# Optimization experiments

Hardware: AMD Instinct MI355X
Metric: run time of the kernel (lower is better)

Reference implementation:

```python
import jax, jax.numpy as jnp
import numpy as np

NUM_EMBEDDINGS = 1024
EMBEDDING_DIM = 256
COMMITMENT_COST = 0.25


def setup_inputs() -> dict:
    key = jax.random.key(0)
    k_z, k_e = jax.random.split(key)
    z = jax.random.normal(k_z, (16, EMBEDDING_DIM, 4096), dtype=jnp.float32)
    # nn.Embedding init: uniform(-1/K, 1/K)
    emb = jax.random.uniform(
        k_e, (NUM_EMBEDDINGS, EMBEDDING_DIM), dtype=jnp.float32,
        minval=-1.0 / NUM_EMBEDDINGS, maxval=1.0 / NUM_EMBEDDINGS)
    return {"z": z, "emb": emb}


def reference(z, emb):
    # z: [B, D, T] -> [B, T, D]
    zt = jnp.transpose(z, (0, 2, 1))
    B, T, D = zt.shape
    flat = zt.reshape(-1, D)  # [N, D]
    dists = (jnp.sum(flat * flat, axis=1, keepdims=True)
             + jnp.sum(emb * emb, axis=1)
             - 2.0 * jnp.matmul(flat, emb.T))
    idx = jnp.argmin(dists, axis=1)          # [N]
    quantized = emb[idx].reshape(B, T, D)    # gather + reshape
    e_latent_loss = jnp.mean((jax.lax.stop_gradient(quantized) - zt) ** 2)
    q_latent_loss = jnp.mean((quantized - jax.lax.stop_gradient(zt)) ** 2)
    loss = q_latent_loss + COMMITMENT_COST * e_latent_loss
    # straight-through estimator
    quantized_st = zt + jax.lax.stop_gradient(quantized - zt)
    return jnp.transpose(quantized_st, (0, 2, 1)), loss
```

## Files before the change

### kernel.cpp

```cpp
#include <hip/hip_runtime.h>
#include <stdint.h>

#define B_   16
#define D_   256
#define T_   4096
#define K_   1024
#define N_   (B_ * T_)
#define BM   32

typedef __attribute__((ext_vector_type(4))) float floatx4;
typedef __attribute__((ext_vector_type(2))) float floatx2;
typedef __attribute__((ext_vector_type(2))) long longx2;

__global__ __launch_bounds__(256) void emb_prep(const float* __restrict__ emb,
                                                uint32_t* __restrict__ embf8,
                                                float* __restrict__ esqh,
                                                float* __restrict__ lossp) {
    int w = threadIdx.x >> 6, lane = threadIdx.x & 63;
    int k = blockIdx.x * 4 + w;
    float4 v = ((const float4*)emb)[k * 64 + lane];
    float a0 = v.x * 1024.f, a1 = v.y * 1024.f, a2 = v.z * 1024.f, a3 = v.w * 1024.f;
    int p = __builtin_amdgcn_cvt_pk_fp8_f32(a0, a1, 0, false);
    p = __builtin_amdgcn_cvt_pk_fp8_f32(a2, a3, p, true);
    int kk = lane >> 3, quad = (lane >> 1) & 3;
    int widx = (k >> 4) * 1024 + (kk >> 1) * 256 + (quad * 16 + (k & 15)) * 4
             + (kk & 1) * 2 + (lane & 1);
    embf8[widx] = (uint32_t)p;
    float ss = a0 * a0 + a1 * a1 + a2 * a2 + a3 * a3;
    #pragma unroll
    for (int off = 32; off; off >>= 1) ss += __shfl_xor(ss, off, 64);
    if (lane == 0) esqh[k] = ss * (0.5f / 1024.f);
    if (blockIdx.x == 0 && threadIdx.x == 0) *lossp = 0.f;
}

__global__ __launch_bounds__(512, 8) void vq_main(const float* __restrict__ z,
                                                  const uint32_t* __restrict__ embf8,
                                                  const float* __restrict__ esqh,
                                                  float* __restrict__ out0,
                                                  float* __restrict__ lossp) {
    __shared__ __align__(16) unsigned char xs[BM * 256];
    __shared__ float wvals[8][16];
    __shared__ int   pidx[BM];
    __shared__ float zred[8];

    int tid  = threadIdx.x;
    int lane = tid & 63, w = tid >> 6;
    int ml   = lane & 15, quad = lane >> 4;
    int blk  = blockIdx.x;
    int b    = blk >> 7;
    int t0   = (blk & 127) * BM;
    const float* zb = z + (size_t)b * (D_ * T_) + t0;

    float zsq = 0.f;
    {
        int t = tid & 31, sl = tid >> 5;
        int hf = (t >> 4) & 1;
        #pragma unroll
        for (int j = 0; j < 2; ++j) {
            int dgrp = sl + 16 * j;
            int d0 = dgrp * 8;
            float f0 = zb[(d0 + 0) * T_ + t];
            float f1 = zb[(d0 + 1) * T_ + t];
            float f2 = zb[(d0 + 2) * T_ + t];
            float f3 = zb[(d0 + 3) * T_ + t];
            float f4 = zb[(d0 + 4) * T_ + t];
            float f5 = zb[(d0 + 5) * T_ + t];
            float f6 = zb[(d0 + 6) * T_ + t];
            float f7 = zb[(d0 + 7) * T_ + t];
            zsq += f0*f0 + f1*f1 + f2*f2 + f3*f3 + f4*f4 + f5*f5 + f6*f6 + f7*f7;
            uint32_t p0 = (uint32_t)__builtin_amdgcn_cvt_pk_fp8_f32(f0, f1, 0, false);
            p0 = (uint32_t)__builtin_amdgcn_cvt_pk_fp8_f32(f2, f3, (int)p0, true);
            uint32_t p1 = (uint32_t)__builtin_amdgcn_cvt_pk_fp8_f32(f4, f5, 0, false);
            p1 = (uint32_t)__builtin_amdgcn_cvt_pk_fp8_f32(f6, f7, (int)p1, true);
            int c = dgrp >> 1, h = dgrp & 1;
            *(uint2*)&xs[t * 256 + ((c ^ (t & 15)) << 4) + ((h ^ hf) << 3)] =
                make_uint2(p0, p1);
        }
    }
    __syncthreads();

    int set = w >> 2;
    long afr[8];
    {
        int pnt = set * 16 + ml;
        #pragma unroll
        for (int kk = 0; kk < 8; ++kk) {
            int c = 2 * kk + (quad >> 1), h = quad & 1;
            afr[kk] = *(const long*)&xs[pnt * 256 + ((c ^ ml) << 4) + ((h ^ (set & 1)) << 3)];
        }
    }

    float bv[4];
    #pragma unroll
    for (int i = 0; i < 4; ++i) bv[i] = 1e30f;

    int ct0 = (w & 3) * 16;
    const char* ebL = (const char*)embf8 + (size_t)ct0 * 4096 + (size_t)lane * 16;
    const float* ehp = esqh + ct0 * 16 + ml;
    const unsigned hi_mask = 0xFFFFFC00u;
    #pragma unroll 1
    for (int j = 0; j < 16; ++j) {
        const char* p = ebL + (size_t)j * 4096;
        longx2 qq[4];
        #pragma unroll
        for (int i = 0; i < 4; ++i)
            qq[i] = *(const longx2*)(p + i * 1024);
        float eh = ehp[j * 16];
        floatx4 a0 = {0.f, 0.f, 0.f, 0.f};
        #pragma unroll
        for (int i = 0; i < 4; ++i) {
            a0 = __builtin_amdgcn_mfma_f32_16x16x32_fp8_fp8(afr[2*i],     qq[i][0], a0, 0, 0, 0);
            a0 = __builtin_amdgcn_mfma_f32_16x16x32_fp8_fp8(afr[2*i + 1], qq[i][1], a0, 0, 0, 0);
        }
        unsigned cbits = (unsigned)((ct0 + j) * 16 + ml);
        #pragma unroll
        for (int i = 0; i < 4; ++i) {
            float dv = eh - a0[i];
            bv[i] = fminf(bv[i], __uint_as_float((__float_as_uint(dv) & hi_mask) | cbits));
        }
    }

    #pragma unroll
    for (int i = 0; i < 4; ++i) {
        float v = bv[i];
        #pragma unroll
        for (int off = 1; off < 16; off <<= 1)
            v = fminf(v, __shfl_xor(v, off, 64));
        if (ml == 0) wvals[w][quad * 4 + i] = v;
    }
    #pragma unroll
    for (int off = 32; off; off >>= 1) zsq += __shfl_xor(zsq, off, 64);
    if (lane == 0) zred[w] = zsq;
    __syncthreads();

    if (tid < 32) {
        int t = tid, qb = (t >> 4) * 4, pis = t & 15;
        float wv = fminf(fminf(wvals[qb][pis], wvals[qb + 1][pis]),
                         fminf(wvals[qb + 2][pis], wvals[qb + 3][pis]));
        pidx[t] = (int)(__float_as_uint(wv) & 1023u);
        float lsum = wv;
        #pragma unroll
        for (int off = 16; off; off >>= 1) lsum += __shfl_xor(lsum, off, 64);
        if (t == 0) {
            float tot = zred[0] + zred[1] + zred[2] + zred[3]
                      + zred[4] + zred[5] + zred[6] + zred[7]
                      + lsum * (2.0f / 1024.f);
            atomicAdd(lossp, tot * (1.25f / 16777216.0f));
        }
    }
    __syncthreads();

    {
        int t = tid >> 4;
        int g = tid & 15;
        int code = pidx[t];
        const char* src = (const char*)embf8 + (size_t)(code >> 4) * 4096
                        + (g >> 2) * 1024 + ((g & 3) * 16 + (code & 15)) * 16;
        uint4 v = *(const uint4*)src;
        *(uint4*)&xs[t * 256 + ((g ^ (t & 15)) << 4)] = v;
    }
    __syncthreads();

    float* ob = out0 + (size_t)b * (D_ * T_) + t0;
    {
        int t = tid & 31, g = tid >> 5;
        uint4 v = *(const uint4*)&xs[t * 256 + ((g ^ (t & 15)) << 4)];
        uint32_t wd[4] = {v.x, v.y, v.z, v.w};
        #pragma unroll
        for (int u = 0; u < 4; ++u) {
            int kk = (g >> 2) * 2 + (u >> 1);
            int d0 = kk * 32 + (g & 3) * 8 + (u & 1) * 4;
            floatx2 lo = __builtin_amdgcn_cvt_pk_f32_fp8((int)wd[u], false);
            floatx2 hi = __builtin_amdgcn_cvt_pk_f32_fp8((int)wd[u], true);
            ob[(d0 + 0) * T_ + t] = lo[0] * (1.f / 1024.f);
            ob[(d0 + 1) * T_ + t] = lo[1] * (1.f / 1024.f);
            ob[(d0 + 2) * T_ + t] = hi[0] * (1.f / 1024.f);
            ob[(d0 + 3) * T_ + t] = hi[1] * (1.f / 1024.f);
        }
    }
}

extern "C" void kernel_launch(void* const* d_in, const int* in_sizes, int n_in,
                              void* d_out, int out_size, void* d_ws, size_t ws_size,
                              hipStream_t stream) {
    (void)in_sizes; (void)n_in; (void)out_size; (void)ws_size;
    const float* z   = (const float*)d_in[0];
    const float* emb = (const float*)d_in[1];

    uint32_t* embf8 = (uint32_t*)d_ws;
    float*    esqh  = (float*)((char*)d_ws + (size_t)K_ * D_);

    float* out0  = (float*)d_out;
    float* lossp = out0 + (size_t)N_ * D_;

    emb_prep<<<K_ / 4, 256, 0, stream>>>(emb, embf8, esqh, lossp);
    vq_main<<<N_ / BM, 512, 0, stream>>>(z, embf8, esqh, out0, lossp);
}
```

Baseline: 159.8 us.

## Keep codebook slice resident in registers and process 128 points per block

Each wave now loads its 128-code slice of the fp8 codebook into registers once (64 longs) and reuses it across eight 16-point tiles. Previously it streamed codebook fragments from global memory for every 32-point block. Each block covers 128 points, with double-buffered A-fragment loads from LDS and independent MFMA accumulators per code tile. The cost is much higher register pressure, with occupancy bounds lowered from 8 to 2 blocks per CU, and a quarter as many blocks.

New measurement: 148.2 us. 7.2% less time.

```diff
diff --git a/kernel.cpp b/kernel.cpp
--- a/kernel.cpp
+++ b/kernel.cpp
@@ -6,7 +6,7 @@
 #define T_   4096
 #define K_   1024
 #define N_   (B_ * T_)
-#define BM   32
+#define BP   128
 
 typedef __attribute__((ext_vector_type(4))) float floatx4;
 typedef __attribute__((ext_vector_type(2))) float floatx2;
@@ -33,31 +33,33 @@
     if (blockIdx.x == 0 && threadIdx.x == 0) *lossp = 0.f;
 }
 
-__global__ __launch_bounds__(512, 8) void vq_main(const float* __restrict__ z,
+__global__ __launch_bounds__(512, 2) void vq_main(const float* __restrict__ z,
                                                   const uint32_t* __restrict__ embf8,
                                                   const float* __restrict__ esqh,
                                                   float* __restrict__ out0,
                                                   float* __restrict__ lossp) {
-    __shared__ __align__(16) unsigned char xs[BM * 256];
-    __shared__ float wvals[8][16];
-    __shared__ int   pidx[BM];
+    __shared__ __align__(16) unsigned char xs[BP * 256];
+    __shared__ float wvals[8][BP];
+    __shared__ int   pidx[BP];
     __shared__ float zred[8];
+    __shared__ float lred[2];
 
     int tid  = threadIdx.x;
     int lane = tid & 63, w = tid >> 6;
     int ml   = lane & 15, quad = lane >> 4;
     int blk  = blockIdx.x;
-    int b    = blk >> 7;
-    int t0   = (blk & 127) * BM;
+    int b    = blk >> 5;
+    int t0   = (blk & 31) * BP;
     const float* zb = z + (size_t)b * (D_ * T_) + t0;
+    float* ob = out0 + (size_t)b * (D_ * T_) + t0;
 
     float zsq = 0.f;
     {
-        int t = tid & 31, sl = tid >> 5;
+        int t = lane + 64 * (w & 1);
         int hf = (t >> 4) & 1;
-        #pragma unroll
-        for (int j = 0; j < 2; ++j) {
-            int dgrp = sl + 16 * j;
+        #pragma unroll 2
+        for (int j = 0; j < 8; ++j) {
+            int dgrp = (w >> 1) + 4 * j;
             int d0 = dgrp * 8;
             float f0 = zb[(d0 + 0) * T_ + t];
             float f1 = zb[(d0 + 1) * T_ + t];
@@ -77,81 +79,112 @@
                 make_uint2(p0, p1);
         }
     }
-    __syncthreads();
-
-    int set = w >> 2;
-    long afr[8];
+
+    long bfr[8][8];
+    float ehr[8];
     {
-        int pnt = set * 16 + ml;
-        #pragma unroll
-        for (int kk = 0; kk < 8; ++kk) {
-            int c = 2 * kk + (quad >> 1), h = quad & 1;
-            afr[kk] = *(const long*)&xs[pnt * 256 + ((c ^ ml) << 4) + ((h ^ (set & 1)) << 3)];
+        const char* ebW = (const char*)embf8 + (size_t)(w * 8) * 4096 + (size_t)lane * 16;
+        #pragma unroll
+        for (int ct = 0; ct < 8; ++ct) {
+            #pragma unroll
+            for (int i = 0; i < 4; ++i) {
+                longx2 q = *(const longx2*)(ebW + ct * 4096 + i * 1024);
+                bfr[ct][2 * i]     = q[0];
+                bfr[ct][2 * i + 1] = q[1];
+            }
+            ehr[ct] = esqh[(w * 8 + ct) * 16 + ml];
         }
     }
-
-    float bv[4];
-    #pragma unroll
-    for (int i = 0; i < 4; ++i) bv[i] = 1e30f;
-
-    int ct0 = (w & 3) * 16;
-    const char* ebL = (const char*)embf8 + (size_t)ct0 * 4096 + (size_t)lane * 16;
-    const float* ehp = esqh + ct0 * 16 + ml;
+    __syncthreads();
+
+    const floatx4 zv = {0.f, 0.f, 0.f, 0.f};
     const unsigned hi_mask = 0xFFFFFC00u;
+    int cb_base = w * 128 + ml;
+
+#define LOAD_AFR(AFR, S)                                                        \
+    {                                                                           \
+        int pnt = (S) * 16 + ml;                                                \
+        _Pragma("unroll")                                                       \
+        for (int kk = 0; kk < 8; ++kk) {                                        \
+            int c = 2 * kk + (quad >> 1), h = quad & 1;                         \
+            AFR[kk] = *(const long*)&xs[pnt * 256 + ((c ^ ml) << 4)             \
+                                        + ((h ^ ((S) & 1)) << 3)];              \
+        }                                                                       \
+    }
+
+#define PT_TILE(AFR, S)                                                         \
+    {                                                                           \
+        floatx4 acc[8];                                                         \
+        _Pragma("unroll")                                                       \
+        for (int ct = 0; ct < 8; ++ct)                                          \
+            acc[ct] = __builtin_amdgcn_mfma_f32_16x16x32_fp8_fp8(AFR[0], bfr[ct][0], zv, 0, 0, 0); \
+        _Pragma("unroll")                                                       \
+        for (int kk = 1; kk < 8; ++kk) {                                        \
+            _Pragma("unroll")                                                   \
+            for (int ct = 0; ct < 8; ++ct)                                      \
+                acc[ct] = __builtin_amdgcn_mfma_f32_16x16x32_fp8_fp8(AFR[kk], bfr[ct][kk], acc[ct], 0, 0, 0); \
+        }                                                                       \
+        float bvr[4] = {1e30f, 1e30f, 1e30f, 1e30f};                            \
+        _Pragma("unroll")                                                       \
+        for (int ct = 0; ct < 8; ++ct) {                                        \
+            unsigned cb = (unsigned)(cb_base + ct * 16);                        \
+            _Pragma("unroll")                                                   \
+            for (int i = 0; i < 4; ++i) {                                       \
+                float dd = ehr[ct] - acc[ct][i];                                \
+                bvr[i] = fminf(bvr[i], __uint_as_float((__float_as_uint(dd) & hi_mask) | cb)); \
+            }                                                                   \
+        }                                                                       \
+        _Pragma("unroll")                                                       \
+        for (int i = 0; i < 4; ++i) {                                           \
+            float v = bvr[i];                                                   \
+            _Pragma("unroll")                                                   \
+            for (int off = 1; off < 16; off <<= 1)                              \
+                v = fminf(v, __shfl_xor(v, off, 64));                           \
+            if (ml == 0) wvals[w][(S) * 16 + quad * 4 + i] = v;                 \
+        }                                                                       \
+    }
+
+    long afrA[8], afrB[8];
+    LOAD_AFR(afrA, 0)
     #pragma unroll 1
-    for (int j = 0; j < 16; ++j) {
-        const char* p = ebL + (size_t)j * 4096;
-        longx2 qq[4];
-        #pragma unroll
-        for (int i = 0; i < 4; ++i)
-            qq[i] = *(const longx2*)(p + i * 1024);
-        float eh = ehp[j * 16];
-        floatx4 a0 = {0.f, 0.f, 0.f, 0.f};
-        #pragma unroll
-        for (int i = 0; i < 4; ++i) {
-            a0 = __builtin_amdgcn_mfma_f32_16x16x32_fp8_fp8(afr[2*i],     qq[i][0], a0, 0, 0, 0);
-            a0 = __builtin_amdgcn_mfma_f32_16x16x32_fp8_fp8(afr[2*i + 1], qq[i][1], a0, 0, 0, 0);
-        }
-        unsigned cbits = (unsigned)((ct0 + j) * 16 + ml);
-        #pragma unroll
-        for (int i = 0; i < 4; ++i) {
-            float dv = eh - a0[i];
-            bv[i] = fminf(bv[i], __uint_as_float((__float_as_uint(dv) & hi_mask) | cbits));
-        }
-    }
-
-    #pragma unroll
-    for (int i = 0; i < 4; ++i) {
-        float v = bv[i];
-        #pragma unroll
-        for (int off = 1; off < 16; off <<= 1)
-            v = fminf(v, __shfl_xor(v, off, 64));
-        if (ml == 0) wvals[w][quad * 4 + i] = v;
-    }
+    for (int s = 0; s < 8; s += 2) {
+        LOAD_AFR(afrB, s + 1)
+        PT_TILE(afrA, s)
+        if (s + 2 < 8) LOAD_AFR(afrA, s + 2)
+        PT_TILE(afrB, s + 1)
+    }
+
+#undef LOAD_AFR
+#undef PT_TILE
+
     #pragma unroll
     for (int off = 32; off; off >>= 1) zsq += __shfl_xor(zsq, off, 64);
     if (lane == 0) zred[w] = zsq;
     __syncthreads();
 
-    if (tid < 32) {
-        int t = tid, qb = (t >> 4) * 4, pis = t & 15;
-        float wv = fminf(fminf(wvals[qb][pis], wvals[qb + 1][pis]),
-                         fminf(wvals[qb + 2][pis], wvals[qb + 3][pis]));
+    if (tid < BP) {
+        int t = tid;
+        float wv = wvals[0][t];
+        #pragma unroll
+        for (int k = 1; k < 8; ++k) wv = fminf(wv, wvals[k][t]);
         pidx[t] = (int)(__float_as_uint(wv) & 1023u);
         float lsum = wv;
         #pragma unroll
-        for (int off = 16; off; off >>= 1) lsum += __shfl_xor(lsum, off, 64);
-        if (t == 0) {
-            float tot = zred[0] + zred[1] + zred[2] + zred[3]
-                      + zred[4] + zred[5] + zred[6] + zred[7]
-                      + lsum * (2.0f / 1024.f);
-            atomicAdd(lossp, tot * (1.25f / 16777216.0f));
-        }
-    }
-    __syncthreads();
-
-    {
-        int t = tid >> 4;
+        for (int off = 32; off; off >>= 1) lsum += __shfl_xor(lsum, off, 64);
+        if ((tid & 63) == 0) lred[tid >> 6] = lsum;
+    }
+    __syncthreads();
+
+    if (tid == 0) {
+        float tot = zred[0] + zred[1] + zred[2] + zred[3]
+                  + zred[4] + zred[5] + zred[6] + zred[7]
+                  + (lred[0] + lred[1]) * (2.0f / 1024.f);
+        atomicAdd(lossp, tot * (1.25f / 16777216.0f));
+    }
+
+    #pragma unroll
+    for (int m = 0; m < 4; ++m) {
+        int t = (tid >> 4) + 32 * m;
         int g = tid & 15;
         int code = pidx[t];
         const char* src = (const char*)embf8 + (size_t)(code >> 4) * 4096
@@ -161,21 +194,24 @@
     }
     __syncthreads();
 
-    float* ob = out0 + (size_t)b * (D_ * T_) + t0;
     {
-        int t = tid & 31, g = tid >> 5;
-        uint4 v = *(const uint4*)&xs[t * 256 + ((g ^ (t & 15)) << 4)];
-        uint32_t wd[4] = {v.x, v.y, v.z, v.w};
-        #pragma unroll
-        for (int u = 0; u < 4; ++u) {
-            int kk = (g >> 2) * 2 + (u >> 1);
-            int d0 = kk * 32 + (g & 3) * 8 + (u & 1) * 4;
-            floatx2 lo = __builtin_amdgcn_cvt_pk_f32_fp8((int)wd[u], false);
-            floatx2 hi = __builtin_amdgcn_cvt_pk_f32_fp8((int)wd[u], true);
-            ob[(d0 + 0) * T_ + t] = lo[0] * (1.f / 1024.f);
-            ob[(d0 + 1) * T_ + t] = lo[1] * (1.f / 1024.f);
-            ob[(d0 + 2) * T_ + t] = hi[0] * (1.f / 1024.f);
-            ob[(d0 + 3) * T_ + t] = hi[1] * (1.f / 1024.f);
+        int t = tid & 127, wq = tid >> 7;
+        #pragma unroll
+        for (int jj = 0; jj < 4; ++jj) {
+            int g = wq + 4 * jj;
+            uint4 v = *(const uint4*)&xs[t * 256 + ((g ^ (t & 15)) << 4)];
+            uint32_t wd[4] = {v.x, v.y, v.z, v.w};
+            #pragma unroll
+            for (int u = 0; u < 4; ++u) {
+                int kk = (g >> 2) * 2 + (u >> 1);
+                int d0 = kk * 32 + (g & 3) * 8 + (u & 1) * 4;
+                floatx2 lo = __builtin_amdgcn_cvt_pk_f32_fp8((int)wd[u], false);
+                floatx2 hi = __builtin_amdgcn_cvt_pk_f32_fp8((int)wd[u], true);
+                ob[(d0 + 0) * T_ + t] = lo[0] * (1.f / 1024.f);
+                ob[(d0 + 1) * T_ + t] = lo[1] * (1.f / 1024.f);
+                ob[(d0 + 2) * T_ + t] = hi[0] * (1.f / 1024.f);
+                ob[(d0 + 3) * T_ + t] = hi[1] * (1.f / 1024.f);
+            }
         }
     }
 }
@@ -194,5 +230,5 @@
     float* lossp = out0 + (size_t)N_ * D_;
 
     emb_prep<<<K_ / 4, 256, 0, stream>>>(emb, embf8, esqh, lossp);
-    vq_main<<<N_ / BM, 512, 0, stream>>>(z, embf8, esqh, out0, lossp);
+    vq_main<<<N_ / BP, 512, 0, stream>>>(z, embf8, esqh, out0, lossp);
 }
```
